# Kernel tuning notes

Hardware: AMD Instinct MI355X
Metric: run time of the kernel (lower is better)

## Reference

```python
import jax, jax.numpy as jnp
import numpy as np

B = 512; S = 6; Q = 2            # meta-batch, n_way*k_shot, n_way*q_query
DIM = 64; IMG = 28; N_WAY = 2
HEADS = 4; HD = DIM // HEADS     # retrieval heads / head dim
EPS = 1e-5


def _pool_mat(inp, out):
    # exact torch AdaptiveAvgPool2d windowing as a matrix [out, inp]
    P = np.zeros((out, inp), np.float32)
    for i in range(out):
        s = (i * inp) // out
        e = -((-(i + 1) * inp) // out)
        P[i, s:e] = 1.0 / (e - s)
    return jnp.asarray(P)

P28 = _pool_mat(IMG, 8)  # 28 -> 8; subsequent 8 -> 8 pools are identity


def _gelu(x):
    return jax.nn.gelu(x, approximate=False)


def _conv(x, w, b):
    y = jax.lax.conv_general_dilated(x, w, (1, 1), ((1, 1), (1, 1)),
                                     dimension_numbers=('NCHW', 'OIHW', 'NCHW'))
    return y + b[None, :, None, None]


def _bn(x, p):
    # p rows: gamma, beta, running_mean, running_var (eval-mode BatchNorm2d)
    g, bt, m, v = p[0], p[1], p[2], p[3]
    sc = g / jnp.sqrt(v + EPS)
    return (x - m[None, :, None, None]) * sc[None, :, None, None] + bt[None, :, None, None]


def _img_in(x, c1w, c1b, bn1, c2w, c2b, bn2, c3w, c3b, bn3, c4w, c4b, bn4, lin_w):
    h = _bn(_conv(x, c1w, c1b), bn1)
    h = jnp.einsum('oi,ncij,pj->ncop', P28, h, P28)   # adaptive avg pool 28x28 -> 8x8
    h = _gelu(h)                                       # dropout is identity in eval
    h = _gelu(_bn(_conv(h, c2w, c2b), bn2))
    h = _gelu(_bn(_conv(h, c3w, c3b), bn3))
    h = _gelu(_bn(_conv(h, c4w, c4b), bn4))            # -> [N,1,8,8]
    h = h.reshape(h.shape[0], -1)                      # [N,64]
    return h @ lin_w.T                                 # Linear(64 -> DIM, no bias)


def _net(x, w1, w2):
    # x: [B,K,D]; w1,w2: [B,D,D] batched fast weights
    h = jnp.einsum('bed,bkd->bke', w1, x)
    ah = _gelu(h)
    y = jnp.einsum('bed,bkd->bke', w2, ah)
    return y, h


def _get_lor(x, w1, w2, r_q, r_k, r_v, r_o, ln_w, ln_b):
    b, k, _ = x.shape
    q, _ = _net(x, w1, w2)
    qh = jnp.einsum('nhd,bkd->bknh', r_q, q)
    sc = jnp.einsum('bknh,rnh->bknr', qh, r_k) / (HD ** 0.5)
    p = jax.nn.softmax(sc, axis=-1)
    lor = jnp.einsum('bknr,rnh->bknh', p, r_v).reshape(b, k, DIM)
    lor = jnp.einsum('de,bkd->bke', r_o, lor)
    z = lor + x
    mu = z.mean(-1, keepdims=True)
    var = ((z - mu) ** 2).mean(-1, keepdims=True)
    return (z - mu) / jnp.sqrt(var + EPS) * ln_w + ln_b


def _forward(query_w, sxs, qxs, inner_lr, c1w, c1b, bn1, c2w, c2b, bn2, c3w, c3b, bn3,
             c4w, c4b, bn4, lin_w, emb, w1, w2, tags, r_q, r_k, r_v, r_o, ln_w, ln_b,
             sys, qys):
    b = query_w.shape[0]
    s = sxs.shape[1]
    q = qxs.shape[1]
    feats = lambda im: _img_in(im.reshape(-1, 1, IMG, IMG), c1w, c1b, bn1, c2w, c2b,
                               bn2, c3w, c3b, bn3, c4w, c4b, bn4, lin_w)
    sx = feats(sxs).reshape(b, s, DIM)
    qx = feats(qxs).reshape(b, q, DIM)
    qe = tags[4]
    w1b = jnp.broadcast_to(w1, (b, DIM, DIM))
    w2b = jnp.broadcast_to(w2, (b, DIM, DIM))
    bound = sx + emb[sys]                                          # [B,S,D]
    # all 4 tag variants for all S shots in one vectorized get_lor call
    inp = (bound[:, :, None, :] + tags[:4][None, None]).reshape(b, s * 4, DIM)
    lors = _get_lor(inp, w1b, w2b, r_q, r_k, r_v, r_o, ln_w, ln_b).reshape(b, s, 4, DIM)
    l1s, r1s, l2s, r2s = lors[:, :, 0], lors[:, :, 1], lors[:, :, 2], lors[:, :, 3]
    qw1 = w1[None] + jnp.einsum('bsl,bsr->blr', l1s, r1s)
    qw2 = w2[None] + jnp.einsum('bsl,bsr->blr', l2s, r2s)
    preds, _ = _net(qx + qe, qw1, qw2)                             # [B,Q,D]
    logits = jnp.einsum('ld,bqd->bql', emb, preds).reshape(-1, N_WAY)
    labels = qys.reshape(-1)
    ls = jax.nn.log_softmax(logits)
    task_loss = -jnp.take_along_axis(ls, labels[:, None], axis=1).mean()
    n_correct = (jnp.argmax(logits, axis=1) == labels).sum()
    return task_loss, n_correct, b * q


def setup_inputs() -> dict:
    key = jax.random.key(0)
    ks = jax.random.split(key, 24)
    rn = lambda i, sh, sc=1.0: sc * jax.random.normal(ks[i], sh, jnp.float32)
    def bnp(i, c):
        k0, k1, k2 = jax.random.split(ks[i], 3)
        return jnp.stack([1.0 + 0.1 * jax.random.normal(k0, (c,)),
                          0.1 * jax.random.normal(k1, (c,)),
                          0.1 * jax.random.normal(k2, (c,)),
                          0.5 + jax.random.uniform(jax.random.fold_in(ks[i], 3), (c,))])
    return {
        'query_w': rn(0, (B, DIM)),
        'sxs': rn(1, (B, S, IMG * IMG)),
        'qxs': rn(2, (B, Q, IMG * IMG)),
        'inner_lr': jnp.float32(0.1),
        'c1w': rn(3, (32, 1, 3, 3), 0.3), 'c1b': rn(4, (32,), 0.1), 'bn1': bnp(5, 32),
        'c2w': rn(6, (32, 32, 3, 3), 0.06), 'c2b': rn(7, (32,), 0.1), 'bn2': bnp(8, 32),
        'c3w': rn(9, (32, 32, 3, 3), 0.06), 'c3b': rn(10, (32,), 0.1), 'bn3': bnp(11, 32),
        'c4w': rn(12, (1, 32, 3, 3), 0.06), 'c4b': rn(13, (1,), 0.1), 'bn4': bnp(14, 1),
        'lin_w': rn(15, (DIM, 64), 0.125),
        'emb': rn(16, (N_WAY, DIM), 0.125),
        'w1': rn(17, (DIM, DIM), 0.125),
        'w2': rn(18, (DIM, DIM), 0.125),
        'tags': rn(19, (8, DIM), 0.125),
        'r_q': rn(20, (HEADS, HD, DIM), 0.125),
        'r_k': rn(21, (16, HEADS, HD), 0.25),
        'r_v': rn(22, (16, HEADS, HD), 0.25),
        'r_o': rn(23, (DIM, DIM), 0.125),
        'ln_w': 0.001 * jnp.ones((DIM,), jnp.float32),
        'ln_b': jnp.zeros((DIM,), jnp.float32),
        'sys': jax.random.randint(jax.random.fold_in(key, 100), (B, S), 0, N_WAY),
        'qys': jax.random.randint(jax.random.fold_in(key, 101), (B, Q), 0, N_WAY),
    }


def reference(query_w, sxs, qxs, inner_lr, c1w, c1b, bn1, c2w, c2b, bn2, c3w, c3b, bn3,
              c4w, c4b, bn4, lin_w, emb, w1, w2, tags, r_q, r_k, r_v, r_o, ln_w, ln_b,
              sys, qys):
    task_loss, n_correct, n_q = _forward(query_w, sxs, qxs, inner_lr, c1w, c1b, bn1,
                                         c2w, c2b, bn2, c3w, c3b, bn3, c4w, c4b, bn4,
                                         lin_w, emb, w1, w2, tags, r_q, r_k, r_v, r_o,
                                         ln_w, ln_b, sys, qys)
    return (task_loss, task_loss, jnp.float32(0.0), n_correct, n_q)
```

## Files before the change

### kernel.cpp

```cpp
#include <hip/hip_runtime.h>
#include <math.h>

constexpr float EPSF = 1e-5f;

constexpr int WS_W1B  = 0;
constexpr int WS_B1   = 1024;
constexpr int WS_W2B  = 1056;
constexpr int WS_W3B  = 5664;
constexpr int WS_W4B  = 10272;
constexpr int WS_B4   = 10416;
constexpr int WS_B2   = 10420;
constexpr int WS_B3   = 10452;
constexpr int WS_HW1  = 10484;
constexpr int WS_HM   = 12788;
constexpr int WS_HW2  = 15092;
constexpr int WS_HROT = 17396;
constexpr int WS_RKB  = 19700;
constexpr int WS_RVT  = 20212;
constexpr int WS_PART = 20724;
constexpr int WS_CNT  = 21748;

using short8 = __attribute__((ext_vector_type(8))) short;
using f32x4  = __attribute__((ext_vector_type(4))) float;

__device__ __forceinline__ float gelu_f(float x) {
    float z  = fabsf(x) * 0.70710678118654752440f;
    float t  = __builtin_amdgcn_rcpf(__builtin_fmaf(0.3275911f, z, 1.0f));
    float p  = t * __builtin_fmaf(t,
                 __builtin_fmaf(t,
                   __builtin_fmaf(t,
                     __builtin_fmaf(t, 1.061405429f, -1.453152027f),
                     1.421413741f),
                   -0.284496736f),
                 0.254829592f);
    float e  = __expf(-z * z);
    float er = __builtin_fmaf(-p, e, 1.0f);
    float s  = copysignf(er, x);
    return 0.5f * x * (1.0f + s);
}
__device__ __forceinline__ unsigned short f2bf(float f) {
    unsigned u = __float_as_uint(f);
    return (unsigned short)((u + 0x7FFFu + ((u >> 16) & 1u)) >> 16);
}
__device__ __forceinline__ float bflo(unsigned u) { return __uint_as_float(u << 16); }
__device__ __forceinline__ float bfhi(unsigned u) { return __uint_as_float(u & 0xffff0000u); }

__global__ void __launch_bounds__(256) precompute_kernel(
    const float* __restrict__ c1w, const float* __restrict__ c1b, const float* __restrict__ bn1,
    const float* __restrict__ c2w, const float* __restrict__ c2b, const float* __restrict__ bn2,
    const float* __restrict__ c3w, const float* __restrict__ c3b, const float* __restrict__ bn3,
    const float* __restrict__ c4w, const float* __restrict__ c4b, const float* __restrict__ bn4,
    const float* __restrict__ w1, const float* __restrict__ w2,
    const float* __restrict__ rq, const float* __restrict__ ro,
    const float* __restrict__ rk, const float* __restrict__ rv,
    float* __restrict__ ws)
{
    const int gid = blockIdx.x * 256 + threadIdx.x;
    const int gsz = gridDim.x * 256;

    if (gid == 0) *((unsigned*)(ws + WS_CNT)) = 0u;

    unsigned short* w1b = (unsigned short*)(ws + WS_W1B);
    for (int v = gid; v < 2048; v += gsz) {
        int c8 = v & 7, colx = (v >> 3) & 15, qd = (v >> 7) & 3, hh = (v >> 9) & 1, kt = v >> 10;
        int tap = kt * 32 + qd * 8 + c8;
        int oc = hh * 16 + colx;
        unsigned short o = 0;
        if (tap < 36) {
            int tt = tap / 6, s = tap - tt * 6;
            float sum = 0.f;
            for (int di = 0; di < 3; ++di) {
                int a = tt - di; if (a < 0 || a > 3) continue;
                for (int dj = 0; dj < 3; ++dj) {
                    int bb = s - dj; if (bb < 0 || bb > 3) continue;
                    sum += c1w[oc * 9 + di * 3 + dj];
                }
            }
            float sc1 = bn1[oc] * rsqrtf(bn1[96 + oc] + EPSF);
            o = f2bf(sum * sc1 * (1.0f / 16.0f));
        }
        w1b[v] = o;
    }
    for (int c = gid; c < 32; c += gsz) {
        float sc1 = bn1[c] * rsqrtf(bn1[96 + c] + EPSF);
        ws[WS_B1 + c] = (c1b[c] - bn1[64 + c]) * sc1 + bn1[32 + c];
        float sc2 = bn2[c] * rsqrtf(bn2[96 + c] + EPSF);
        ws[WS_B2 + c] = (c2b[c] - bn2[64 + c]) * sc2 + bn2[32 + c];
        float sc3 = bn3[c] * rsqrtf(bn3[96 + c] + EPSF);
        ws[WS_B3 + c] = (c3b[c] - bn3[64 + c]) * sc3 + bn3[32 + c];
    }
    unsigned short* w2b = (unsigned short*)(ws + WS_W2B);
    unsigned short* w3b = (unsigned short*)(ws + WS_W3B);
    for (int v = gid; v < 9216; v += gsz) {
        int c8 = v & 7, colx = (v >> 3) & 15, qd = (v >> 7) & 3, hh = (v >> 9) & 1, tap = v >> 10;
        int oc = hh * 16 + colx;
        int ic = qd * 8 + c8;
        float sc2 = bn2[oc] * rsqrtf(bn2[96 + oc] + EPSF);
        float sc3 = bn3[oc] * rsqrtf(bn3[96 + oc] + EPSF);
        w2b[v] = f2bf(c2w[oc * 288 + ic * 9 + tap] * sc2);
        w3b[v] = f2bf(c3w[oc * 288 + ic * 9 + tap] * sc3);
    }
    {
        unsigned short* w4b = (unsigned short*)(ws + WS_W4B);
        float sc4 = bn4[0] * rsqrtf(bn4[3] + EPSF);
        for (int v = gid; v < 288; v += gsz) {
            int tap = v >> 5, ic = v & 31;
            w4b[v] = f2bf(c4w[ic * 9 + tap] * sc4);
        }
        if (gid == 0) ws[WS_B4] = (c4b[0] - bn4[2]) * sc4 + bn4[1];
    }
    unsigned short* hw1 = (unsigned short*)(ws + WS_HW1);
    unsigned short* hm  = (unsigned short*)(ws + WS_HM);
    unsigned short* hw2 = (unsigned short*)(ws + WS_HW2);
    unsigned short* hro = (unsigned short*)(ws + WS_HROT);
    for (int v = gid; v < 4608; v += gsz) {
        int e = v / 72, d = v - e * 72;
        unsigned short a = 0, b = 0, c = 0, r = 0;
        if (d < 64) {
            a = f2bf(w1[e * 64 + d]);
            b = f2bf(w2[e * 64 + d]);
            float m = 0.f;
            for (int q = 0; q < 64; ++q) m += rq[e * 64 + q] * w2[q * 64 + d];
            c = f2bf(m);
            r = f2bf(ro[d * 64 + e]);
        }
        hw1[v] = a; hw2[v] = b; hm[v] = c; hro[v] = r;
    }
    unsigned short* rkb = (unsigned short*)(ws + WS_RKB);
    unsigned short* rvt = (unsigned short*)(ws + WS_RVT);
    for (int v = gid; v < 1024; v += gsz) {
        int nn = v >> 8, x = (v >> 4) & 15, y = v & 15;
        rkb[v] = f2bf(rk[x * 64 + nn * 16 + y] * 0.25f);
        rvt[v] = f2bf(rv[y * 64 + nn * 16 + x]);
    }
}

struct FeatsSmem {
    unsigned short sAct[8][3200];
    float          sh4[8][64];
};
struct HeadSmem {
    unsigned short sW1B[4608];
    unsigned short sM[4608];
    unsigned short sW2B[4608];
    unsigned short sROT[4608];
    unsigned short bufA[2304];
    unsigned short bufB[2304];
    unsigned short sP[2048];
};
union FusedSmem {
    FeatsSmem f;
    HeadSmem  h;
};

__device__ __forceinline__ void conv32g(const unsigned short* __restrict__ A,
                                        const unsigned short* __restrict__ Wg,
                                        int col, int quad, f32x4 (&acc)[4][2])
{
    int ab[4];
    #pragma unroll
    for (int mt = 0; mt < 4; ++mt) {
        int px = mt * 16 + col;
        ab[mt] = quad * 800 + ((px >> 3) * 10 + (px & 7)) * 8;
        acc[mt][0] = (f32x4){0,0,0,0};
        acc[mt][1] = (f32x4){0,0,0,0};
    }
    #pragma unroll
    for (int dr = 0; dr < 3; ++dr)
        #pragma unroll
        for (int dc = 0; dc < 3; ++dc) {
            int tap = dr * 3 + dc;
            short8 b0 = *(const short8*)(Wg + (((tap * 2 + 0) * 4 + quad) * 16 + col) * 8);
            short8 b1 = *(const short8*)(Wg + (((tap * 2 + 1) * 4 + quad) * 16 + col) * 8);
            #pragma unroll
            for (int mt = 0; mt < 4; ++mt) {
                short8 a = *(const short8*)(A + ab[mt] + (dr * 10 + dc) * 8);
                acc[mt][0] = __builtin_amdgcn_mfma_f32_16x16x32_bf16(a, b0, acc[mt][0], 0, 0, 0);
                acc[mt][1] = __builtin_amdgcn_mfma_f32_16x16x32_bf16(a, b1, acc[mt][1], 0, 0, 0);
            }
        }
}

__device__ __forceinline__ void conv_store4(unsigned short* __restrict__ A,
                                            const f32x4 (&acc)[4][2],
                                            float bi0, float bi1, int col, int quad)
{
    #pragma unroll
    for (int mt = 0; mt < 4; ++mt)
        #pragma unroll
        for (int reg = 0; reg < 4; ++reg) {
            int px = mt * 16 + quad * 4 + reg;
            int P = ((px >> 3) + 1) * 10 + (px & 7) + 1;
            A[(col >> 3) * 800 + P * 8 + (col & 7)]       = f2bf(gelu_f(acc[mt][0][reg] + bi0));
            A[(2 + (col >> 3)) * 800 + P * 8 + (col & 7)] = f2bf(gelu_f(acc[mt][1][reg] + bi1));
        }
}

__device__ __forceinline__ f32x4 head_gemm8(const unsigned short* __restrict__ Ab,
                                            const unsigned short* __restrict__ Bw,
                                            int col, int quad, int wvid)
{
    int mt = wvid & 1, nt = wvid >> 1;
    f32x4 acc = {0, 0, 0, 0};
    #pragma unroll
    for (int kt = 0; kt < 2; ++kt) {
        short8 a = *(const short8*)(Ab + (mt * 16 + col) * 72 + kt * 32 + quad * 8);
        short8 b = *(const short8*)(Bw + (nt * 16 + col) * 72 + kt * 32 + quad * 8);
        acc = __builtin_amdgcn_mfma_f32_16x16x32_bf16(a, b, acc, 0, 0, 0);
    }
    return acc;
}

__global__ void __launch_bounds__(512, 4) fused_kernel(
    const float* __restrict__ sxs, const float* __restrict__ qxs,
    const float* __restrict__ lin_w,
    const float* __restrict__ emb, const float* __restrict__ tags,
    const float* __restrict__ lnw, const float* __restrict__ lnb,
    const int* __restrict__ sys, const int* __restrict__ qys,
    float* __restrict__ ws, float* __restrict__ out)
{
    __shared__ __align__(16) FusedSmem sm;
    __shared__ __align__(16) float sFeat[8][64];
    __shared__ __align__(16) float sXf[1536];
    __shared__ __align__(16) float s_xq[128], s_ah[128], s_yp[128];
    __shared__ float s_t1[12], s_t2[12], s_mu[24], s_rs[24], s_lg[4], s_red[16];
    __shared__ int s_last;

    const int t    = threadIdx.x;
    const int b    = blockIdx.x;
    const int wv   = t >> 6;
    const int lane = t & 63;
    const int col  = lane & 15;
    const int quad = lane >> 4;

    {
        unsigned short* A = sm.f.sAct[wv];
        float bi1a = ws[WS_B1 + col], bi1b = ws[WS_B1 + 16 + col];
        float bi2a = ws[WS_B2 + col], bi2b = ws[WS_B2 + 16 + col];
        float bi3a = ws[WS_B3 + col], bi3b = ws[WS_B3 + 16 + col];
        float b4   = ws[WS_B4];

        {
            const float* img = (wv < 6) ? (sxs + ((size_t)b * 6 + wv) * 784)
                                        : (qxs + ((size_t)b * 2 + (wv - 6)) * 784);
            const float4* sv = (const float4*)img;
            #pragma unroll
            for (int j = 0; j < 4; ++j) {
                int idx = j * 64 + lane;
                if (idx < 196) {
                    float4 v = sv[idx];
                    ushort4 o = { f2bf(v.x), f2bf(v.y), f2bf(v.z), f2bf(v.w) };
                    *(ushort4*)(A + idx * 4) = o;
                }
            }
        }

        f32x4 acc[4][2];
        {
            const unsigned short* w1g = (const unsigned short*)(ws + WS_W1B);
            short8 b00 = *(const short8*)(w1g + ((0 * 4 + quad) * 16 + col) * 8);
            short8 b01 = *(const short8*)(w1g + ((1 * 4 + quad) * 16 + col) * 8);
            short8 b10 = *(const short8*)(w1g + ((2 * 4 + quad) * 16 + col) * 8);
            short8 b11 = *(const short8*)(w1g + ((3 * 4 + quad) * 16 + col) * 8);
            int ttj[8], ssj[8];
            #pragma unroll
            for (int j = 0; j < 8; ++j) {
                int k = quad * 8 + j;
                ttj[j] = k / 6; ssj[j] = k - ttj[j] * 6;
            }
            #pragma unroll
            for (int mt = 0; mt < 4; ++mt) {
                acc[mt][0] = (f32x4){0,0,0,0};
                acc[mt][1] = (f32x4){0,0,0,0};
                int px = mt * 16 + col;
                int sr = (((px >> 3) * 7) >> 1) - 1;
                int sc = (((px & 7) * 7) >> 1) - 1;
                short8 a0;
                #pragma unroll
                for (int j = 0; j < 8; ++j) {
                    int rr = sr + ttj[j], cc = sc + ssj[j];
                    bool ok = ((unsigned)rr < 28u) && ((unsigned)cc < 28u);
                    int off = ok ? (rr * 28 + cc) : 0;
                    unsigned short hv = A[off];
                    a0[j] = ok ? (short)hv : (short)0;
                }
                acc[mt][0] = __builtin_amdgcn_mfma_f32_16x16x32_bf16(a0, b00, acc[mt][0], 0, 0, 0);
                acc[mt][1] = __builtin_amdgcn_mfma_f32_16x16x32_bf16(a0, b01, acc[mt][1], 0, 0, 0);
                short8 a1 = {0,0,0,0,0,0,0,0};
                if (quad == 0) {
                    #pragma unroll
                    for (int j = 0; j < 4; ++j) {
                        int rr = sr + 5, cc = sc + 2 + j;
                        bool ok = ((unsigned)rr < 28u) && ((unsigned)cc < 28u);
                        int off = ok ? (rr * 28 + cc) : 0;
                        unsigned short hv = A[off];
                        a1[j] = ok ? (short)hv : (short)0;
                    }
                }
                acc[mt][0] = __builtin_amdgcn_mfma_f32_16x16x32_bf16(a1, b10, acc[mt][0], 0, 0, 0);
                acc[mt][1] = __builtin_amdgcn_mfma_f32_16x16x32_bf16(a1, b11, acc[mt][1], 0, 0, 0);
            }
        }
        {
            uint4 z4 = {0, 0, 0, 0};
            #pragma unroll
            for (int it = 0; it < 3; ++it) {
                int h = lane + it * 64;
                if (h < 144) {
                    int pi = h >> 2, ch = h & 3;
                    int P;
                    if (pi < 10)      P = pi;
                    else if (pi < 20) P = 90 + (pi - 10);
                    else { int k = pi - 20; int r = 1 + (k >> 1); P = r * 10 + (k & 1) * 9; }
                    ((uint4*)A)[ch * 100 + P] = z4;
                }
            }
        }
        conv_store4(A, acc, bi1a, bi1b, col, quad);

        conv32g(A, (const unsigned short*)(ws + WS_W2B), col, quad, acc);
        conv_store4(A, acc, bi2a, bi2b, col, quad);
        conv32g(A, (const unsigned short*)(ws + WS_W3B), col, quad, acc);
        conv_store4(A, acc, bi3a, bi3b, col, quad);

        {
            f32x4 acc4[4];
            int ab[4];
            #pragma unroll
            for (int mt = 0; mt < 4; ++mt) {
                int px = mt * 16 + col;
                ab[mt] = quad * 800 + ((px >> 3) * 10 + (px & 7)) * 8;
                acc4[mt] = (f32x4){0,0,0,0};
            }
            const unsigned short* w4g = (const unsigned short*)(ws + WS_W4B);
            #pragma unroll
            for (int dr = 0; dr < 3; ++dr)
                #pragma unroll
                for (int dc = 0; dc < 3; ++dc) {
                    int tap = dr * 3 + dc;
                    short8 bb = *(const short8*)(w4g + tap * 32 + quad * 8);
                    #pragma unroll
                    for (int mt = 0; mt < 4; ++mt) {
                        short8 a = *(const short8*)(A + ab[mt] + (dr * 10 + dc) * 8);
                        acc4[mt] = __builtin_amdgcn_mfma_f32_16x16x32_bf16(a, bb, acc4[mt], 0, 0, 0);
                    }
                }
            if (col < 4) {
                f32x4 v = acc4[0];
                if (col == 1) v = acc4[1];
                else if (col == 2) v = acc4[2];
                else if (col == 3) v = acc4[3];
                #pragma unroll
                for (int reg = 0; reg < 4; ++reg)
                    sm.f.sh4[wv][col * 16 + quad * 4 + reg] = gelu_f(v[reg] + b4);
            }
        }
        {
            const float4* lw = (const float4*)(lin_w + (size_t)lane * 64);
            const float4* hp = (const float4*)sm.f.sh4[wv];
            float acc2 = 0.f;
            #pragma unroll
            for (int j = 0; j < 16; ++j) {
                float4 w = lw[j], h = hp[j];
                acc2 += w.x * h.x + w.y * h.y + w.z * h.z + w.w * h.w;
            }
            sFeat[wv][lane] = acc2;
        }
    }
    __syncthreads();

    for (int i = t; i < 576; i += 512) {
        ((uint4*)sm.h.sW1B)[i] = ((const uint4*)(ws + WS_HW1))[i];
        ((uint4*)sm.h.sM)[i]   = ((const uint4*)(ws + WS_HM))[i];
        ((uint4*)sm.h.sW2B)[i] = ((const uint4*)(ws + WS_HW2))[i];
        ((uint4*)sm.h.sROT)[i] = ((const uint4*)(ws + WS_HROT))[i];
    }
    if (t < 72) {
        uint4 z = {0, 0, 0, 0};
        ((uint4*)(sm.h.bufA + 1728))[t] = z;
        ((uint4*)(sm.h.bufB + 1728))[t] = z;
    }
    for (int idx = t; idx < 1536; idx += 512) {
        int k = idx >> 6, e = idx & 63;
        int s = k >> 2, tg = k & 3;
        int cls = sys[b * 6 + s];
        float v = sFeat[s][e] + emb[cls * 64 + e] + tags[tg * 64 + e];
        sXf[idx] = v;
        sm.h.bufA[k * 72 + e] = f2bf(v);
    }
    if (t < 128) {
        int q = t >> 6, e = t & 63;
        s_xq[t] = sFeat[6 + q][e] + tags[256 + e];
    }
    __syncthreads();

    {
        f32x4 r = head_gemm8(sm.h.bufA, sm.h.sW1B, col, quad, wv);
        int mt = wv & 1, nt = wv >> 1;
        #pragma unroll
        for (int reg = 0; reg < 4; ++reg) {
            int row = mt * 16 + quad * 4 + reg;
            if (row < 24) sm.h.bufB[row * 72 + nt * 16 + col] = f2bf(gelu_f(r[reg]));
        }
    }
    __syncthreads();
    {
        f32x4 r = head_gemm8(sm.h.bufB, sm.h.sM, col, quad, wv);
        int mt = wv & 1, nt = wv >> 1;
        #pragma unroll
        for (int reg = 0; reg < 4; ++reg) {
            int row = mt * 16 + quad * 4 + reg;
            if (row < 24) sm.h.bufA[row * 72 + nt * 16 + col] = f2bf(r[reg]);
        }
    }
    __syncthreads();

    if (wv < 4) {
        const int nh = wv;
        const unsigned short* rkB = (const unsigned short*)(ws + WS_RKB) + nh * 256;
        const unsigned short* rvT = (const unsigned short*)(ws + WS_RVT) + nh * 256;
        unsigned short* bufA = sm.h.bufA;
        unsigned short* sP   = sm.h.sP;
        const short8 zz = {0,0,0,0,0,0,0,0};
        const bool lo = (quad < 2);
        {
            int r8 = lane >> 3, c2 = lane & 7;
            *(unsigned int*)(sP + (24 + r8) * 64 + nh * 16 + c2 * 2) = 0u;
        }
        short8 bK = lo ? *(const short8*)(rkB + col * 16 + quad * 8) : zz;
        short8 a0 = lo ? *(const short8*)(bufA + col * 72 + nh * 16 + quad * 8) : zz;
        short8 a1 = lo ? *(const short8*)(bufA + (16 + col) * 72 + nh * 16 + quad * 8) : zz;
        f32x4 s0 = __builtin_amdgcn_mfma_f32_16x16x32_bf16(a0, bK, (f32x4){0,0,0,0}, 0, 0, 0);
        f32x4 s1 = __builtin_amdgcn_mfma_f32_16x16x32_bf16(a1, bK, (f32x4){0,0,0,0}, 0, 0, 0);
        #pragma unroll
        for (int reg = 0; reg < 4; ++reg) {
            float v = s0[reg];
            float m = v;
            m = fmaxf(m, __shfl_xor(m, 1)); m = fmaxf(m, __shfl_xor(m, 2));
            m = fmaxf(m, __shfl_xor(m, 4)); m = fmaxf(m, __shfl_xor(m, 8));
            float p = __expf(v - m);
            float su = p;
            su += __shfl_xor(su, 1); su += __shfl_xor(su, 2);
            su += __shfl_xor(su, 4); su += __shfl_xor(su, 8);
            sP[(quad * 4 + reg) * 64 + nh * 16 + col] = f2bf(p / su);
            v = s1[reg];
            m = v;
            m = fmaxf(m, __shfl_xor(m, 1)); m = fmaxf(m, __shfl_xor(m, 2));
            m = fmaxf(m, __shfl_xor(m, 4)); m = fmaxf(m, __shfl_xor(m, 8));
            p = __expf(v - m);
            su = p;
            su += __shfl_xor(su, 1); su += __shfl_xor(su, 2);
            su += __shfl_xor(su, 4); su += __shfl_xor(su, 8);
            if (quad < 2) sP[(16 + quad * 4 + reg) * 64 + nh * 16 + col] = f2bf(p / su);
        }
        short8 bV  = lo ? *(const short8*)(rvT + col * 16 + quad * 8) : zz;
        short8 pa0 = lo ? *(const short8*)(sP + col * 64 + nh * 16 + quad * 8) : zz;
        short8 pa1 = lo ? *(const short8*)(sP + (16 + col) * 64 + nh * 16 + quad * 8) : zz;
        f32x4 o0 = __builtin_amdgcn_mfma_f32_16x16x32_bf16(pa0, bV, (f32x4){0,0,0,0}, 0, 0, 0);
        f32x4 o1 = __builtin_amdgcn_mfma_f32_16x16x32_bf16(pa1, bV, (f32x4){0,0,0,0}, 0, 0, 0);
        #pragma unroll
        for (int reg = 0; reg < 4; ++reg) {
            bufA[(quad * 4 + reg) * 72 + nh * 16 + col] = f2bf(o0[reg]);
            int tok = 16 + quad * 4 + reg;
            if (tok < 24) bufA[tok * 72 + nh * 16 + col] = f2bf(o1[reg]);
        }
    }
    __syncthreads();

    {
        f32x4 r = head_gemm8(sm.h.bufA, sm.h.sROT, col, quad, wv);
        int mt = wv & 1, nt = wv >> 1;
        #pragma unroll
        for (int reg = 0; reg < 4; ++reg) {
            int row = mt * 16 + quad * 4 + reg;
            if (row < 24) {
                int idx = row * 64 + nt * 16 + col;
                sXf[idx] = sXf[idx] + r[reg];
            }
        }
    }
    __syncthreads();

    if (t < 192) {
        int k = t >> 3, j = t & 7;
        const float4* zp = (const float4*)(sXf + k * 64 + j * 8);
        float4 v0 = zp[0], v1 = zp[1];
        float sx_ = v0.x + v0.y + v0.z + v0.w + v1.x + v1.y + v1.z + v1.w;
        sx_ += __shfl_xor(sx_, 1); sx_ += __shfl_xor(sx_, 2); sx_ += __shfl_xor(sx_, 4);
        float mu = sx_ * (1.0f / 64.0f);
        float d0 = v0.x - mu, d1 = v0.y - mu, d2 = v0.z - mu, d3 = v0.w - mu;
        float d4 = v1.x - mu, d5 = v1.y - mu, d6 = v1.z - mu, d7 = v1.w - mu;
        float vv = d0*d0 + d1*d1 + d2*d2 + d3*d3 + d4*d4 + d5*d5 + d6*d6 + d7*d7;
        vv += __shfl_xor(vv, 1); vv += __shfl_xor(vv, 2); vv += __shfl_xor(vv, 4);
        if (j == 0) {
            s_mu[k] = mu;
            s_rs[k] = 1.0f / sqrtf(vv * (1.0f / 64.0f) + EPSF);
        }
    }
    __syncthreads();
    for (int idx = t; idx < 1536; idx += 512) {
        int k = idx >> 6, e = idx & 63;
        float v = (sXf[idx] - s_mu[k]) * s_rs[k] * lnw[e] + lnb[e];
        sm.h.bufB[k * 72 + e] = f2bf(v);
    }
    __syncthreads();

    if (t < 96) {
        int idx = t >> 3, j = t & 7;
        int q = idx / 6, s = idx - q * 6;
        uint4 u = ((const uint4*)(sm.h.bufB + (s * 4 + 1) * 72))[j];
        const float* x = s_xq + q * 64 + j * 8;
        float d = bflo(u.x)*x[0] + bfhi(u.x)*x[1] + bflo(u.y)*x[2] + bfhi(u.y)*x[3]
                + bflo(u.z)*x[4] + bfhi(u.z)*x[5] + bflo(u.w)*x[6] + bfhi(u.w)*x[7];
        d += __shfl_xor(d, 1); d += __shfl_xor(d, 2); d += __shfl_xor(d, 4);
        if (j == 0) s_t1[idx] = d;
    }
    __syncthreads();
    if (t < 128) {
        int q = t >> 6, e = t & 63;
        const uint4* wp = (const uint4*)(sm.h.sW1B + e * 72);
        const float* xp = s_xq + q * 64;
        float acc = 0.f;
        #pragma unroll
        for (int j = 0; j < 8; ++j) {
            uint4 u = wp[j];
            const float* x = xp + j * 8;
            acc += bflo(u.x)*x[0] + bfhi(u.x)*x[1] + bflo(u.y)*x[2] + bfhi(u.y)*x[3]
                 + bflo(u.z)*x[4] + bfhi(u.z)*x[5] + bflo(u.w)*x[6] + bfhi(u.w)*x[7];
        }
        #pragma unroll
        for (int s = 0; s < 6; ++s)
            acc += bflo((unsigned)sm.h.bufB[(s * 4 + 0) * 72 + e]) * s_t1[q * 6 + s];
        s_ah[t] = gelu_f(acc);
    }
    __syncthreads();
    if (t < 96) {
        int idx = t >> 3, j = t & 7;
        int q = idx / 6, s = idx - q * 6;
        uint4 u = ((const uint4*)(sm.h.bufB + (s * 4 + 3) * 72))[j];
        const float* x = s_ah + q * 64 + j * 8;
        float d = bflo(u.x)*x[0] + bfhi(u.x)*x[1] + bflo(u.y)*x[2] + bfhi(u.y)*x[3]
                + bflo(u.z)*x[4] + bfhi(u.z)*x[5] + bflo(u.w)*x[6] + bfhi(u.w)*x[7];
        d += __shfl_xor(d, 1); d += __shfl_xor(d, 2); d += __shfl_xor(d, 4);
        if (j == 0) s_t2[idx] = d;
    }
    __syncthreads();
    if (t < 128) {
        int q = t >> 6, e = t & 63;
        const uint4* wp = (const uint4*)(sm.h.sW2B + e * 72);
        const float* xp = s_ah + q * 64;
        float acc = 0.f;
        #pragma unroll
        for (int j = 0; j < 8; ++j) {
            uint4 u = wp[j];
            const float* x = xp + j * 8;
            acc += bflo(u.x)*x[0] + bfhi(u.x)*x[1] + bflo(u.y)*x[2] + bfhi(u.y)*x[3]
                 + bflo(u.z)*x[4] + bfhi(u.z)*x[5] + bflo(u.w)*x[6] + bfhi(u.w)*x[7];
        }
        #pragma unroll
        for (int s = 0; s < 6; ++s)
            acc += bflo((unsigned)sm.h.bufB[(s * 4 + 2) * 72 + e]) * s_t2[q * 6 + s];
        s_yp[t] = acc;
    }
    __syncthreads();

    float* part = ws + WS_PART;
    if (t < 32) {
        int q = t >> 4, ll = (t >> 3) & 1, j = t & 7;
        const float* ep = emb + ll * 64 + j * 8;
        const float* yp = s_yp + q * 64 + j * 8;
        float d = ep[0]*yp[0] + ep[1]*yp[1] + ep[2]*yp[2] + ep[3]*yp[3]
                + ep[4]*yp[4] + ep[5]*yp[5] + ep[6]*yp[6] + ep[7]*yp[7];
        d += __shfl_xor(d, 1); d += __shfl_xor(d, 2); d += __shfl_xor(d, 4);
        if (j == 0) s_lg[q * 2 + ll] = d;
    }
    if (t == 0) {
        float lsum = 0.f, corr = 0.f;
        #pragma unroll
        for (int q = 0; q < 2; ++q) {
            float l0 = s_lg[q * 2], l1 = s_lg[q * 2 + 1];
            int lab = qys[b * 2 + q];
            float m = fmaxf(l0, l1);
            float lse = m + logf(expf(l0 - m) + expf(l1 - m));
            lsum += -((lab ? l1 : l0) - lse);
            int pred = (l1 > l0) ? 1 : 0;
            corr += (pred == lab) ? 1.0f : 0.0f;
        }
        part[b] = lsum;
        part[512 + b] = corr;
        __threadfence();
        unsigned old = atomicAdd((unsigned*)(ws + WS_CNT), 1u);
        s_last = (old == 511) ? 1 : 0;
    }
    __syncthreads();

    if (s_last) {
        __threadfence();
        float l = part[t];
        float c = part[512 + t];
        #pragma unroll
        for (int off = 1; off < 64; off <<= 1) {
            l += __shfl_xor(l, off);
            c += __shfl_xor(c, off);
        }
        if (lane == 0) { s_red[wv * 2] = l; s_red[wv * 2 + 1] = c; }
        __syncthreads();
        if (t == 0) {
            float L = 0.f, C = 0.f;
            #pragma unroll
            for (int w = 0; w < 8; ++w) { L += s_red[w * 2]; C += s_red[w * 2 + 1]; }
            float loss = L * (1.0f / 1024.0f);
            out[0] = loss;
            out[1] = loss;
            out[2] = 0.0f;
            out[3] = C;
            out[4] = 1024.0f;
        }
    }
}

extern "C" void kernel_launch(void* const* d_in, const int* in_sizes, int n_in,
                              void* d_out, int out_size, void* d_ws, size_t ws_size,
                              hipStream_t stream)
{
    (void)in_sizes; (void)n_in; (void)out_size; (void)ws_size;
    const float* sxs  = (const float*)d_in[1];
    const float* qxs  = (const float*)d_in[2];
    const float* c1w  = (const float*)d_in[4];
    const float* c1b  = (const float*)d_in[5];
    const float* bn1  = (const float*)d_in[6];
    const float* c2w  = (const float*)d_in[7];
    const float* c2b  = (const float*)d_in[8];
    const float* bn2  = (const float*)d_in[9];
    const float* c3w  = (const float*)d_in[10];
    const float* c3b  = (const float*)d_in[11];
    const float* bn3  = (const float*)d_in[12];
    const float* c4w  = (const float*)d_in[13];
    const float* c4b  = (const float*)d_in[14];
    const float* bn4  = (const float*)d_in[15];
    const float* lin_w= (const float*)d_in[16];
    const float* emb  = (const float*)d_in[17];
    const float* w1   = (const float*)d_in[18];
    const float* w2   = (const float*)d_in[19];
    const float* tags = (const float*)d_in[20];
    const float* rq   = (const float*)d_in[21];
    const float* rk   = (const float*)d_in[22];
    const float* rv   = (const float*)d_in[23];
    const float* ro   = (const float*)d_in[24];
    const float* lnw  = (const float*)d_in[25];
    const float* lnb  = (const float*)d_in[26];
    const int*   sys  = (const int*)d_in[27];
    const int*   qys  = (const int*)d_in[28];

    float* ws  = (float*)d_ws;
    float* out = (float*)d_out;

    precompute_kernel<<<64, 256, 0, stream>>>(c1w, c1b, bn1, c2w, c2b, bn2,
                                              c3w, c3b, bn3, c4w, c4b, bn4,
                                              w1, w2, rq, ro, rk, rv, ws);
    fused_kernel<<<512, 512, 0, stream>>>(sxs, qxs, lin_w, emb, tags, lnw, lnb,
                                          sys, qys, ws, out);
}
```

Measured before the change: 174.0 us.

## Read head weights from global, fuse feature assembly and layernorm, pad activation stride

```diff
diff --git a/kernel.cpp b/kernel.cpp
--- a/kernel.cpp
+++ b/kernel.cpp
@@ -20,6 +20,9 @@
 constexpr int WS_PART = 20724;
 constexpr int WS_CNT  = 21748;
 
+constexpr int ACT_CS  = 816;
+constexpr int ACT_SZ  = 4 * ACT_CS;
+
 using short8 = __attribute__((ext_vector_type(8))) short;
 using f32x4  = __attribute__((ext_vector_type(4))) float;
 
@@ -136,16 +139,10 @@
 }
 
 struct FeatsSmem {
-    unsigned short sAct[8][3200];
+    unsigned short sAct[8][ACT_SZ];
     float          sh4[8][64];
 };
 struct HeadSmem {
-    unsigned short sW1B[4608];
-    unsigned short sM[4608];
-    unsigned short sW2B[4608];
-    unsigned short sROT[4608];
-    unsigned short bufA[2304];
-    unsigned short bufB[2304];
     unsigned short sP[2048];
 };
 union FusedSmem {
@@ -161,7 +158,7 @@
     #pragma unroll
     for (int mt = 0; mt < 4; ++mt) {
         int px = mt * 16 + col;
-        ab[mt] = quad * 800 + ((px >> 3) * 10 + (px & 7)) * 8;
+        ab[mt] = quad * ACT_CS + ((px >> 3) * 10 + (px & 7)) * 8;
         acc[mt][0] = (f32x4){0,0,0,0};
         acc[mt][1] = (f32x4){0,0,0,0};
     }
@@ -191,8 +188,8 @@
         for (int reg = 0; reg < 4; ++reg) {
             int px = mt * 16 + quad * 4 + reg;
             int P = ((px >> 3) + 1) * 10 + (px & 7) + 1;
-            A[(col >> 3) * 800 + P * 8 + (col & 7)]       = f2bf(gelu_f(acc[mt][0][reg] + bi0));
-            A[(2 + (col >> 3)) * 800 + P * 8 + (col & 7)] = f2bf(gelu_f(acc[mt][1][reg] + bi1));
+            A[(col >> 3) * ACT_CS + P * 8 + (col & 7)]       = f2bf(gelu_f(acc[mt][0][reg] + bi0));
+            A[(2 + (col >> 3)) * ACT_CS + P * 8 + (col & 7)] = f2bf(gelu_f(acc[mt][1][reg] + bi1));
         }
 }
 
@@ -220,10 +217,10 @@
     float* __restrict__ ws, float* __restrict__ out)
 {
     __shared__ __align__(16) FusedSmem sm;
-    __shared__ __align__(16) float sFeat[8][64];
+    __shared__ __align__(16) unsigned short bufA[2304], bufB[2304];
     __shared__ __align__(16) float sXf[1536];
     __shared__ __align__(16) float s_xq[128], s_ah[128], s_yp[128];
-    __shared__ float s_t1[12], s_t2[12], s_mu[24], s_rs[24], s_lg[4], s_red[16];
+    __shared__ float s_t1[12], s_t2[12], s_lg[4], s_red[16];
     __shared__ int s_last;
 
     const int t    = threadIdx.x;
@@ -232,6 +229,23 @@
     const int lane = t & 63;
     const int col  = lane & 15;
     const int quad = lane >> 4;
+
+    float embv = 0.f, tg0 = 0.f, tg1 = 0.f, tg2 = 0.f, tg3 = 0.f, tgq = 0.f;
+    if (wv < 6) {
+        int cls = sys[b * 6 + wv];
+        embv = emb[cls * 64 + lane];
+        tg0 = tags[0 * 64 + lane];
+        tg1 = tags[1 * 64 + lane];
+        tg2 = tags[2 * 64 + lane];
+        tg3 = tags[3 * 64 + lane];
+    } else {
+        tgq = tags[256 + lane];
+    }
+    if (t < 72) {
+        uint4 z = {0, 0, 0, 0};
+        ((uint4*)(bufA + 1728))[t] = z;
+        ((uint4*)(bufB + 1728))[t] = z;
+    }
 
     {
         unsigned short* A = sm.f.sAct[wv];
@@ -312,7 +326,7 @@
                     if (pi < 10)      P = pi;
                     else if (pi < 20) P = 90 + (pi - 10);
                     else { int k = pi - 20; int r = 1 + (k >> 1); P = r * 10 + (k & 1) * 9; }
-                    ((uint4*)A)[ch * 100 + P] = z4;
+                    ((uint4*)A)[ch * (ACT_CS / 8) + P] = z4;
                 }
             }
         }
@@ -329,7 +343,7 @@
             #pragma unroll
             for (int mt = 0; mt < 4; ++mt) {
                 int px = mt * 16 + col;
-                ab[mt] = quad * 800 + ((px >> 3) * 10 + (px & 7)) * 8;
+                ab[mt] = quad * ACT_CS + ((px >> 3) * 10 + (px & 7)) * 8;
                 acc4[mt] = (f32x4){0,0,0,0};
             }
             const unsigned short* w4g = (const unsigned short*)(ws + WS_W4B);
@@ -364,53 +378,46 @@
                 float4 w = lw[j], h = hp[j];
                 acc2 += w.x * h.x + w.y * h.y + w.z * h.z + w.w * h.w;
             }
-            sFeat[wv][lane] = acc2;
-        }
-    }
-    __syncthreads();
-
-    for (int i = t; i < 576; i += 512) {
-        ((uint4*)sm.h.sW1B)[i] = ((const uint4*)(ws + WS_HW1))[i];
-        ((uint4*)sm.h.sM)[i]   = ((const uint4*)(ws + WS_HM))[i];
-        ((uint4*)sm.h.sW2B)[i] = ((const uint4*)(ws + WS_HW2))[i];
-        ((uint4*)sm.h.sROT)[i] = ((const uint4*)(ws + WS_HROT))[i];
-    }
-    if (t < 72) {
-        uint4 z = {0, 0, 0, 0};
-        ((uint4*)(sm.h.bufA + 1728))[t] = z;
-        ((uint4*)(sm.h.bufB + 1728))[t] = z;
-    }
-    for (int idx = t; idx < 1536; idx += 512) {
-        int k = idx >> 6, e = idx & 63;
-        int s = k >> 2, tg = k & 3;
-        int cls = sys[b * 6 + s];
-        float v = sFeat[s][e] + emb[cls * 64 + e] + tags[tg * 64 + e];
-        sXf[idx] = v;
-        sm.h.bufA[k * 72 + e] = f2bf(v);
-    }
-    if (t < 128) {
-        int q = t >> 6, e = t & 63;
-        s_xq[t] = sFeat[6 + q][e] + tags[256 + e];
-    }
-    __syncthreads();
+            if (wv < 6) {
+                float base = acc2 + embv;
+                float v0 = base + tg0, v1 = base + tg1, v2 = base + tg2, v3 = base + tg3;
+                sXf[(wv * 4 + 0) * 64 + lane] = v0;
+                sXf[(wv * 4 + 1) * 64 + lane] = v1;
+                sXf[(wv * 4 + 2) * 64 + lane] = v2;
+                sXf[(wv * 4 + 3) * 64 + lane] = v3;
+                bufA[(wv * 4 + 0) * 72 + lane] = f2bf(v0);
+                bufA[(wv * 4 + 1) * 72 + lane] = f2bf(v1);
+                bufA[(wv * 4 + 2) * 72 + lane] = f2bf(v2);
+                bufA[(wv * 4 + 3) * 72 + lane] = f2bf(v3);
+            } else {
+                s_xq[(wv - 6) * 64 + lane] = acc2 + tgq;
+            }
+        }
+    }
+    __syncthreads();
+
+    const unsigned short* gW1 = (const unsigned short*)(ws + WS_HW1);
+    const unsigned short* gM  = (const unsigned short*)(ws + WS_HM);
+    const unsigned short* gW2 = (const unsigned short*)(ws + WS_HW2);
+    const unsigned short* gRO = (const unsigned short*)(ws + WS_HROT);
 
     {
-        f32x4 r = head_gemm8(sm.h.bufA, sm.h.sW1B, col, quad, wv);
+        f32x4 r = head_gemm8(bufA, gW1, col, quad, wv);
         int mt = wv & 1, nt = wv >> 1;
         #pragma unroll
         for (int reg = 0; reg < 4; ++reg) {
             int row = mt * 16 + quad * 4 + reg;
-            if (row < 24) sm.h.bufB[row * 72 + nt * 16 + col] = f2bf(gelu_f(r[reg]));
+            if (row < 24) bufB[row * 72 + nt * 16 + col] = f2bf(gelu_f(r[reg]));
         }
     }
     __syncthreads();
     {
-        f32x4 r = head_gemm8(sm.h.bufB, sm.h.sM, col, quad, wv);
+        f32x4 r = head_gemm8(bufB, gM, col, quad, wv);
         int mt = wv & 1, nt = wv >> 1;
         #pragma unroll
         for (int reg = 0; reg < 4; ++reg) {
             int row = mt * 16 + quad * 4 + reg;
-            if (row < 24) sm.h.bufA[row * 72 + nt * 16 + col] = f2bf(r[reg]);
+            if (row < 24) bufA[row * 72 + nt * 16 + col] = f2bf(r[reg]);
         }
     }
     __syncthreads();
@@ -419,8 +426,7 @@
         const int nh = wv;
         const unsigned short* rkB = (const unsigned short*)(ws + WS_RKB) + nh * 256;
         const unsigned short* rvT = (const unsigned short*)(ws + WS_RVT) + nh * 256;
-        unsigned short* bufA = sm.h.bufA;
-        unsigned short* sP   = sm.h.sP;
+        unsigned short* sP = sm.h.sP;
         const short8 zz = {0,0,0,0,0,0,0,0};
         const bool lo = (quad < 2);
         {
@@ -468,7 +474,7 @@
     __syncthreads();
 
     {
-        f32x4 r = head_gemm8(sm.h.bufA, sm.h.sROT, col, quad, wv);
+        f32x4 r = head_gemm8(bufA, gRO, col, quad, wv);
         int mt = wv & 1, nt = wv >> 1;
         #pragma unroll
         for (int reg = 0; reg < 4; ++reg) {
@@ -492,23 +498,23 @@
         float d4 = v1.x - mu, d5 = v1.y - mu, d6 = v1.z - mu, d7 = v1.w - mu;
         float vv = d0*d0 + d1*d1 + d2*d2 + d3*d3 + d4*d4 + d5*d5 + d6*d6 + d7*d7;
         vv += __shfl_xor(vv, 1); vv += __shfl_xor(vv, 2); vv += __shfl_xor(vv, 4);
-        if (j == 0) {
-            s_mu[k] = mu;
-            s_rs[k] = 1.0f / sqrtf(vv * (1.0f / 64.0f) + EPSF);
-        }
-    }
-    __syncthreads();
-    for (int idx = t; idx < 1536; idx += 512) {
-        int k = idx >> 6, e = idx & 63;
-        float v = (sXf[idx] - s_mu[k]) * s_rs[k] * lnw[e] + lnb[e];
-        sm.h.bufB[k * 72 + e] = f2bf(v);
+        float rs = 1.0f / sqrtf(vv * (1.0f / 64.0f) + EPSF);
+        const float4* lwv = (const float4*)(lnw + j * 8);
+        const float4* lbv = (const float4*)(lnb + j * 8);
+        float4 w0 = lwv[0], w1_ = lwv[1], b0 = lbv[0], b1_ = lbv[1];
+        ushort4 o0 = { f2bf(d0 * rs * w0.x + b0.x), f2bf(d1 * rs * w0.y + b0.y),
+                       f2bf(d2 * rs * w0.z + b0.z), f2bf(d3 * rs * w0.w + b0.w) };
+        ushort4 o1 = { f2bf(d4 * rs * w1_.x + b1_.x), f2bf(d5 * rs * w1_.y + b1_.y),
+                       f2bf(d6 * rs * w1_.z + b1_.z), f2bf(d7 * rs * w1_.w + b1_.w) };
+        *(ushort4*)(bufB + k * 72 + j * 8)     = o0;
+        *(ushort4*)(bufB + k * 72 + j * 8 + 4) = o1;
     }
     __syncthreads();
 
     if (t < 96) {
         int idx = t >> 3, j = t & 7;
         int q = idx / 6, s = idx - q * 6;
-        uint4 u = ((const uint4*)(sm.h.bufB + (s * 4 + 1) * 72))[j];
+        uint4 u = ((const uint4*)(bufB + (s * 4 + 1) * 72))[j];
         const float* x = s_xq + q * 64 + j * 8;
         float d = bflo(u.x)*x[0] + bfhi(u.x)*x[1] + bflo(u.y)*x[2] + bfhi(u.y)*x[3]
                 + bflo(u.z)*x[4] + bfhi(u.z)*x[5] + bflo(u.w)*x[6] + bfhi(u.w)*x[7];
@@ -518,7 +524,7 @@
     __syncthreads();
     if (t < 128) {
         int q = t >> 6, e = t & 63;
-        const uint4* wp = (const uint4*)(sm.h.sW1B + e * 72);
+        const uint4* wp = (const uint4*)(gW1 + e * 72);
         const float* xp = s_xq + q * 64;
         float acc = 0.f;
         #pragma unroll
@@ -530,14 +536,14 @@
         }
         #pragma unroll
         for (int s = 0; s < 6; ++s)
-            acc += bflo((unsigned)sm.h.bufB[(s * 4 + 0) * 72 + e]) * s_t1[q * 6 + s];
+            acc += bflo((unsigned)bufB[(s * 4 + 0) * 72 + e]) * s_t1[q * 6 + s];
         s_ah[t] = gelu_f(acc);
     }
     __syncthreads();
     if (t < 96) {
         int idx = t >> 3, j = t & 7;
         int q = idx / 6, s = idx - q * 6;
-        uint4 u = ((const uint4*)(sm.h.bufB + (s * 4 + 3) * 72))[j];
+        uint4 u = ((const uint4*)(bufB + (s * 4 + 3) * 72))[j];
         const float* x = s_ah + q * 64 + j * 8;
         float d = bflo(u.x)*x[0] + bfhi(u.x)*x[1] + bflo(u.y)*x[2] + bfhi(u.y)*x[3]
                 + bflo(u.z)*x[4] + bfhi(u.z)*x[5] + bflo(u.w)*x[6] + bfhi(u.w)*x[7];
@@ -547,7 +553,7 @@
     __syncthreads();
     if (t < 128) {
         int q = t >> 6, e = t & 63;
-        const uint4* wp = (const uint4*)(sm.h.sW2B + e * 72);
+        const uint4* wp = (const uint4*)(gW2 + e * 72);
         const float* xp = s_ah + q * 64;
         float acc = 0.f;
         #pragma unroll
@@ -559,7 +565,7 @@
         }
         #pragma unroll
         for (int s = 0; s < 6; ++s)
-            acc += bflo((unsigned)sm.h.bufB[(s * 4 + 2) * 72 + e]) * s_t2[q * 6 + s];
+            acc += bflo((unsigned)bufB[(s * 4 + 2) * 72 + e]) * s_t2[q * 6 + s];
         s_yp[t] = acc;
     }
     __syncthreads();
```

New measurement: 171.3 us. About the same (-1.6%).
